# Performance work log

Hardware: AMD Instinct MI355X
Metric: run time of the kernel (lower is better)

Reference implementation:

```python
import jax, jax.numpy as jnp
import numpy as np

WS = 8  # window size (hardcoded in original forward)

def _window_partition(x, ws=WS):
    b, c, h, w = x.shape
    ph = (-h) % ws
    pw = (-w) % ws
    x = jnp.pad(x, ((0, 0), (0, 0), (0, ph), (0, pw)), mode='reflect')
    H, W = h + ph, w + pw
    # matches torch .view(b,c,ws,H//ws,ws,W//ws).permute(0,1,2,4,3,5)
    x = x.reshape(b, c, ws, H // ws, ws, W // ws)
    x = x.transpose(0, 1, 2, 4, 3, 5).reshape(b, c * ws * ws, H // ws, W // ws)
    return x, h, w, c, H // ws

def _l2norm_dim1(x):
    # F.normalize(x, p=2) defaults to dim=1 (token axis for [b, L, d]), eps=1e-12
    n = jnp.sqrt(jnp.sum(x * x, axis=1, keepdims=True))
    return x / jnp.maximum(n, 1e-12)

def _forward(q, k, v):
    b = q.shape[0]
    qp, qh, qw, qc, patch = _window_partition(q)
    kp, _, _, _, _ = _window_partition(k)
    vp, _, _, _, _ = _window_partition(v)
    d = qp.shape[1]  # c * ws * ws
    qt = qp.transpose(0, 2, 3, 1).reshape(b, -1, d)  # [b, L, d]
    kt = kp.transpose(0, 2, 3, 1).reshape(b, -1, d)
    vt = vp.transpose(0, 2, 3, 1).reshape(b, -1, d)
    _q = _l2norm_dim1(qt)
    _k = _l2norm_dim1(kt)
    _v = _l2norm_dim1(vt)
    sim = jnp.einsum('bld,bmd->blm', _q, _k) * (d ** -0.5)  # [b, L, L]
    out = jnp.einsum('blm,bmd->bld', jax.nn.softmax(sim, axis=-1), _v)
    # window_reverse
    L = out.shape[1]
    ws = WS
    x = out.reshape(b, patch, L // patch, qc, ws, ws)
    x = x.transpose(0, 3, 4, 1, 5, 2)  # (b, c, ws, patch, ws, L//patch)
    H = ws * patch
    x = x.reshape(b, qc, H, -1)
    return x[:, :, :qh, :qw]

def setup_inputs() -> dict:
    key = jax.random.key(0)
    kq, kk, kv = jax.random.split(key, 3)
    shape = (8, 32, 252, 252)
    return {
        'q': jax.random.normal(kq, shape, dtype=jnp.float32),
        'k': jax.random.normal(kk, shape, dtype=jnp.float32),
        'v': jax.random.normal(kv, shape, dtype=jnp.float32),
    }

def reference(q, k, v):
    return _forward(q, k, v)
```

## Files before the change

### kernel.cpp

```cpp
#include <hip/hip_runtime.h>
#include <cstdint>
#include <cstddef>


typedef __bf16 bf16x8 __attribute__((ext_vector_type(8)));
typedef float  f32x4  __attribute__((ext_vector_type(4)));

__device__ __forceinline__ unsigned int f2bf(float f) {
  unsigned int u = __builtin_bit_cast(unsigned int, f);
  u += 0x7FFFu + ((u >> 16) & 1u);
  return u >> 16;
}
__device__ __forceinline__ float bf2f(unsigned int h) {
  return __builtin_bit_cast(float, h << 16);
}

__device__ __forceinline__ void load_lds16(const void* g, void* l) {
  __builtin_amdgcn_global_load_lds(
      (const __attribute__((address_space(1))) void*)g,
      (__attribute__((address_space(3))) void*)l, 16, 0, 0);
}

__global__ __launch_bounds__(512)
void pack_qk_fused(const float* __restrict__ q, const float* __restrict__ k,
                   unsigned short* __restrict__ Qh,
                   unsigned short* __restrict__ Kh) {
  int bx  = blockIdx.x;
  int t   = bx >> 9;
  int b   = (bx >> 6) & 7;
  int i0  = (bx >> 3) & 7;
  int j0  = bx & 7;
  const float* xb = (t ? k : q) + (size_t)b * 32 * 63504;

  __shared__ unsigned short tile[1024 * 36];
  __shared__ float red[512];
  __shared__ float sclt[32];

  int tid = threadIdx.x;
  int ch  = tid & 7;
  int i1h = (tid >> 3) & 1;
  int c   = tid >> 4;

  int wbase = j0 * 32 + ch * 4;
  float we[4];
  #pragma unroll
  for (int e = 0; e < 4; e++) {
    int w = wbase + e;
    we[e] = (w >= 252) ? 0.f : (((unsigned)(w - 247) <= 3u) ? 2.f : 1.f);
  }
  bool tail = (wbase == 252);

  float pa = 0.f;
  unsigned short* X = (t ? Kh : Qh) + (size_t)b * 1024 * 2048;
  const float* csrc = xb + (size_t)c * 63504;

  #pragma unroll 4
  for (int r = 0; r < 16; r++) {
    int i1 = i1h * 16 + r;
    int h  = i0 * 32 + i1;
    int hs = (h < 252) ? h : 502 - h;
    float rw = (h >= 252) ? 0.f : (((unsigned)(h - 247) <= 3u) ? 2.f : 1.f);
    const float* rowp = csrc + (size_t)hs * 252;

    float4 vv;
    if (!tail) {
      vv = *(const float4*)&rowp[wbase];
    } else {
      vv.x = rowp[250]; vv.y = rowp[249]; vv.z = rowp[248]; vv.w = rowp[247];
    }
    pa += rw * (we[0] * vv.x * vv.x + we[1] * vv.y * vv.y +
                we[2] * vv.z * vv.z + we[3] * vv.w * vv.w);
    int lbase = i1 * 32 + ch * 4;
    unsigned short* tp = &tile[(size_t)lbase * 36 + c];
    tp[0]   = (unsigned short)f2bf(vv.x);
    tp[36]  = (unsigned short)f2bf(vv.y);
    tp[72]  = (unsigned short)f2bf(vv.z);
    tp[108] = (unsigned short)f2bf(vv.w);
  }
  __syncthreads();

  red[tid] = pa;
  __syncthreads();
  if (tid < 32) {
    float s = 0.f;
    #pragma unroll
    for (int u = 0; u < 16; u++) s += red[tid * 16 + u];
    sclt[tid] = 1.f / fmaxf(sqrtf(s), 1e-12f);
  }
  __syncthreads();

  {
    int qd   = tid & 7;
    int lidx = tid >> 3;
    float sc[4];
    #pragma unroll
    for (int m = 0; m < 4; m++) sc[m] = sclt[qd * 4 + m];
    unsigned short* Xb = &X[i0 * 256 + j0 * 32 + qd * 4];
    #pragma unroll 4
    for (int it = 0; it < 16; it++) {
      int l = it * 64 + lidx;
      uint2 u = *(const uint2*)&tile[(size_t)l * 36 + qd * 4];
      uint2 o2;
      o2.x = f2bf(bf2f(u.x & 0xFFFF) * sc[0]) |
             (f2bf(bf2f(u.x >> 16)   * sc[1]) << 16);
      o2.y = f2bf(bf2f(u.y & 0xFFFF) * sc[2]) |
             (f2bf(bf2f(u.y >> 16)   * sc[3]) << 16);
      *(uint2*)&Xb[(size_t)l * 2048] = o2;
    }
  }
}

__global__ void pack_v_kernel(const float* __restrict__ v,
                              unsigned short* __restrict__ Vt,
                              float* __restrict__ svsum) {
  int bx = blockIdx.x;
  int b  = bx >> 8;
  int i0 = (bx >> 5) & 7;
  int i1 = bx & 31;
  int h  = i0 * 32 + i1;
  int hs = (h < 252) ? h : 502 - h;
  const float* src = v + (size_t)b * 32 * 63504 + (size_t)hs * 252;
  unsigned short* dst = Vt + (size_t)b * 2048 * 1024
                           + (size_t)(i0 * 256) * 1024 + i1 * 32;

  int tid = threadIdx.x;
  int j1c = tid & 3;
  int c   = (tid >> 2) & 31;
  int j0g = tid >> 7;
  const float* s = src + (size_t)c * 63504;

  float psum[4];

  #pragma unroll
  for (int jj = 0; jj < 4; jj++) {
    int j0 = j0g * 4 + jj;
    int w0 = j0 * 32 + j1c * 8;
    float f0, f1, f2, f3, f4, f5, f6, f7;
    if (w0 + 8 <= 252) {
      float4 a = *(const float4*)&s[w0];
      float4 bq = *(const float4*)&s[w0 + 4];
      f0 = a.x; f1 = a.y; f2 = a.z; f3 = a.w;
      f4 = bq.x; f5 = bq.y; f6 = bq.z; f7 = bq.w;
    } else {
      float4 a = *(const float4*)&s[244];
      float4 bq = *(const float4*)&s[248];
      f0 = bq.x; f1 = bq.y; f2 = bq.z; f3 = bq.w;
      f4 = bq.z; f5 = bq.y; f6 = bq.x; f7 = a.w;
    }
    psum[jj] = f0*f0 + f1*f1 + f2*f2 + f3*f3 + f4*f4 + f5*f5 + f6*f6 + f7*f7;
    uint4 o;
    o.x = f2bf(f0) | (f2bf(f1) << 16);
    o.y = f2bf(f2) | (f2bf(f3) << 16);
    o.z = f2bf(f4) | (f2bf(f5) << 16);
    o.w = f2bf(f6) | (f2bf(f7) << 16);
    *(uint4*)&dst[(size_t)(j0 * 32 + c) * 1024 + j1c * 8] = o;
  }

  #pragma unroll
  for (int jj = 0; jj < 4; jj++) {
    float ssum = psum[jj];
    ssum += __shfl_down(ssum, 2, 4);
    ssum += __shfl_down(ssum, 1, 4);
    if (j1c == 0) {
      int j0 = j0g * 4 + jj;
      atomicAdd(&svsum[(size_t)b * 2048 + i0 * 256 + j0 * 32 + c], ssum);
    }
  }
}

template <int MODE>
__global__ __launch_bounds__(256, 4)
void gemm_nt(const unsigned short* __restrict__ A,
             const unsigned short* __restrict__ B,
             int K, int Asb, int Bsb, void* __restrict__ Cout, float scale,
             const float* __restrict__ sv) {
  __shared__ unsigned short lA[128 * 64];
  __shared__ unsigned short lB[128 * 64];
  __shared__ float svb[(MODE == 1) ? 128 : 1];

  const int flat = blockIdx.x;
  const int zz   = flat & 7;
  const int rr   = flat >> 3;
  const int my   = rr >> 3;
  const int nx   = rr & 7;

  const int tid  = threadIdx.x;
  const int lane = tid & 63;
  const int wave = tid >> 6;
  const int ln15 = lane & 15;
  const int q4   = lane >> 4;
  const int wm   = wave >> 1;
  const int wn   = wave & 1;
  const int m0   = my * 128;
  const int n0   = nx * 128;
  const unsigned short* Ab = A + (size_t)zz * Asb;
  const unsigned short* Bb = B + (size_t)zz * Bsb;

  if (MODE == 1 && tid < 128)
    svb[tid] = 1.f / fmaxf(sqrtf(sv[(size_t)zz * 2048 + m0 + tid]), 1e-12f);

  const int srow = lane >> 3;
  const int kcp  = lane & 7;
  const int kcl  = kcp ^ srow;

  f32x4 acc[4][4] = {};

  for (int k0 = 0; k0 < K; k0 += 64) {
    #pragma unroll
    for (int r = 0; r < 4; r++) {
      int rowg = wave * 32 + r * 8;
      int row  = rowg + srow;
      load_lds16(&Ab[(size_t)(m0 + row) * K + k0 + kcl * 8], &lA[rowg * 64]);
      load_lds16(&Bb[(size_t)(n0 + row) * K + k0 + kcl * 8], &lB[rowg * 64]);
    }
    __syncthreads();
    #pragma unroll
    for (int kk = 0; kk < 2; kk++) {
      bf16x8 af[4], bfr[4];
      #pragma unroll
      for (int mt = 0; mt < 4; mt++) {
        int row = wm * 64 + mt * 16 + ln15;
        int pc  = (kk * 4 + q4) ^ (row & 7);
        af[mt] = *(const bf16x8*)&lA[row * 64 + pc * 8];
      }
      #pragma unroll
      for (int nt = 0; nt < 4; nt++) {
        int row = wn * 64 + nt * 16 + ln15;
        int pc  = (kk * 4 + q4) ^ (row & 7);
        bfr[nt] = *(const bf16x8*)&lB[row * 64 + pc * 8];
      }
      #pragma unroll
      for (int mt = 0; mt < 4; mt++)
        #pragma unroll
        for (int nt = 0; nt < 4; nt++)
          acc[mt][nt] = __builtin_amdgcn_mfma_f32_16x16x32_bf16(
              af[mt], bfr[nt], acc[mt][nt], 0, 0, 0);
    }
    __syncthreads();
  }

  if (MODE == 0) {
    unsigned short* Sb = (unsigned short*)Cout + (size_t)zz * 1024 * 1024;
    #pragma unroll
    for (int mt = 0; mt < 4; mt++) {
      #pragma unroll
      for (int nt = 0; nt < 4; nt++) {
        int col = n0 + wn * 64 + nt * 16 + ln15;
        #pragma unroll
        for (int rg = 0; rg < 4; rg++) {
          int rowi = m0 + wm * 64 + mt * 16 + q4 * 4 + rg;
          Sb[(size_t)rowi * 1024 + col] = (unsigned short)f2bf(acc[mt][nt][rg] * scale);
        }
      }
    }
  } else {
    float* Ob = (float*)Cout;
    #pragma unroll
    for (int mt = 0; mt < 4; mt++) {
      #pragma unroll
      for (int nt = 0; nt < 4; nt++) {
        int l  = n0 + wn * 64 + nt * 16 + ln15;
        int i1 = l >> 5, j1 = l & 31;
        #pragma unroll
        for (int rg = 0; rg < 4; rg++) {
          int rloc = wm * 64 + mt * 16 + q4 * 4 + rg;
          int dp = m0 + rloc;
          int c  = dp & 31;
          int j0 = (dp >> 5) & 7;
          int i0 = dp >> 8;
          int h = i0 * 32 + i1;
          int w = j0 * 32 + j1;
          if (h < 252 && w < 252)
            Ob[(((size_t)zz * 32 + c) * 252 + h) * 252 + w] =
                acc[mt][nt][rg] * svb[rloc];
        }
      }
    }
  }
}

__global__ void softmax_kernel(unsigned short* __restrict__ S) {
  unsigned short* row = S + (size_t)blockIdx.x * 1024;
  int tid  = threadIdx.x;
  int lane = tid & 63;
  int wid  = tid >> 6;

  uint2 u = *(const uint2*)&row[tid * 4];
  float x0 = bf2f(u.x & 0xFFFF);
  float x1 = bf2f(u.x >> 16);
  float x2 = bf2f(u.y & 0xFFFF);
  float x3 = bf2f(u.y >> 16);

  __shared__ float red[8];
  float mx = fmaxf(fmaxf(x0, x1), fmaxf(x2, x3));
  #pragma unroll
  for (int off = 32; off > 0; off >>= 1) mx = fmaxf(mx, __shfl_down(mx, off));
  if (lane == 0) red[wid] = mx;
  __syncthreads();
  if (tid == 0)
    red[4] = fmaxf(fmaxf(red[0], red[1]), fmaxf(red[2], red[3]));
  __syncthreads();
  float bm = red[4];

  float e0 = __expf(x0 - bm), e1 = __expf(x1 - bm);
  float e2 = __expf(x2 - bm), e3 = __expf(x3 - bm);
  float s = e0 + e1 + e2 + e3;
  #pragma unroll
  for (int off = 32; off > 0; off >>= 1) s += __shfl_down(s, off);
  if (lane == 0) red[wid] = s;
  __syncthreads();
  if (tid == 0) red[5] = 1.0f / (red[0] + red[1] + red[2] + red[3]);
  __syncthreads();
  float inv = red[5];

  unsigned int o0 = f2bf(e0 * inv) | (f2bf(e1 * inv) << 16);
  unsigned int o1 = f2bf(e2 * inv) | (f2bf(e3 * inv) << 16);
  uint2 o; o.x = o0; o.y = o1;
  *(uint2*)&row[tid * 4] = o;
}

extern "C" void kernel_launch(void* const* d_in, const int* in_sizes, int n_in,
                              void* d_out, int out_size, void* d_ws, size_t ws_size,
                              hipStream_t stream) {
  const float* q = (const float*)d_in[0];
  const float* k = (const float*)d_in[1];
  const float* v = (const float*)d_in[2];
  float* out = (float*)d_out;

  char* ws = (char*)d_ws;
  float* sv = (float*)ws;
  unsigned short* Qh = (unsigned short*)(ws + 196608);
  unsigned short* Kh = Qh + (size_t)8 * 1024 * 2048;
  unsigned short* Vt = Kh + (size_t)8 * 1024 * 2048;
  unsigned short* S  = Vt + (size_t)8 * 2048 * 1024;

  const float SIM_SCALE = 0.02209708691207961f;

  hipMemsetAsync(sv, 0, (size_t)8 * 2048 * sizeof(float), stream);
  pack_qk_fused<<<1024, 512, 0, stream>>>(q, k, Qh, Kh);
  pack_v_kernel<<<2048, 256, 0, stream>>>(v, Vt, sv);
  gemm_nt<0><<<512, 256, 0, stream>>>(
      Qh, Kh, 2048, 1024 * 2048, 1024 * 2048, (void*)S, SIM_SCALE, nullptr);
  softmax_kernel<<<8192, 256, 0, stream>>>(S);
  gemm_nt<1><<<1024, 256, 0, stream>>>(
      Vt, S, 1024, 2048 * 1024, 1024 * 1024, (void*)out, 1.0f, sv);
}
```

Baseline: 356.3 us.

## Fuse softmax into QK^T GEMM epilogue and defer normalization to PV GEMM

Removes the standalone softmax kernel. The QK^T GEMM epilogue now writes exp(scaled score) without max subtraction and accumulates per-row sums with shuffles plus atomics. The PV GEMM divides its outputs by those row sums in its own epilogue. This saves one full read and write pass over the 8x1024x1024 score matrix and a kernel launch. In exchange it relies on scores being bounded, which holds here because the inputs are L2-normalized and scaled, and it adds atomic contention on the row-sum buffer.

```diff
diff --git a/kernel.cpp b/kernel.cpp
--- a/kernel.cpp
+++ b/kernel.cpp
@@ -173,10 +173,11 @@
 void gemm_nt(const unsigned short* __restrict__ A,
              const unsigned short* __restrict__ B,
              int K, int Asb, int Bsb, void* __restrict__ Cout, float scale,
-             const float* __restrict__ sv) {
+             const float* __restrict__ sv, float* __restrict__ rs) {
   __shared__ unsigned short lA[128 * 64];
   __shared__ unsigned short lB[128 * 64];
   __shared__ float svb[(MODE == 1) ? 128 : 1];
+  __shared__ float rsb[(MODE == 1) ? 128 : 1];
 
   const int flat = blockIdx.x;
   const int zz   = flat & 7;
@@ -196,8 +197,10 @@
   const unsigned short* Ab = A + (size_t)zz * Asb;
   const unsigned short* Bb = B + (size_t)zz * Bsb;
 
-  if (MODE == 1 && tid < 128)
+  if (MODE == 1 && tid < 128) {
     svb[tid] = 1.f / fmaxf(sqrtf(sv[(size_t)zz * 2048 + m0 + tid]), 1e-12f);
+    rsb[tid] = 1.f / rs[(size_t)zz * 1024 + n0 + tid];
+  }
 
   const int srow = lane >> 3;
   const int kcp  = lane & 7;
@@ -244,13 +247,22 @@
     #pragma unroll
     for (int mt = 0; mt < 4; mt++) {
       #pragma unroll
-      for (int nt = 0; nt < 4; nt++) {
-        int col = n0 + wn * 64 + nt * 16 + ln15;
+      for (int rg = 0; rg < 4; rg++) {
+        int rowi = m0 + wm * 64 + mt * 16 + q4 * 4 + rg;
+        float s = 0.f;
         #pragma unroll
-        for (int rg = 0; rg < 4; rg++) {
-          int rowi = m0 + wm * 64 + mt * 16 + q4 * 4 + rg;
-          Sb[(size_t)rowi * 1024 + col] = (unsigned short)f2bf(acc[mt][nt][rg] * scale);
+        for (int nt = 0; nt < 4; nt++) {
+          float e = __expf(acc[mt][nt][rg] * scale);
+          s += e;
+          int col = n0 + wn * 64 + nt * 16 + ln15;
+          Sb[(size_t)rowi * 1024 + col] = (unsigned short)f2bf(e);
         }
+        s += __shfl_xor(s, 1, 16);
+        s += __shfl_xor(s, 2, 16);
+        s += __shfl_xor(s, 4, 16);
+        s += __shfl_xor(s, 8, 16);
+        if (ln15 == 0)
+          atomicAdd(&rs[(size_t)zz * 1024 + rowi], s);
       }
     }
   } else {
@@ -259,8 +271,10 @@
     for (int mt = 0; mt < 4; mt++) {
       #pragma unroll
       for (int nt = 0; nt < 4; nt++) {
-        int l  = n0 + wn * 64 + nt * 16 + ln15;
+        int lcol = wn * 64 + nt * 16 + ln15;
+        int l  = n0 + lcol;
         int i1 = l >> 5, j1 = l & 31;
+        float rv = rsb[lcol];
         #pragma unroll
         for (int rg = 0; rg < 4; rg++) {
           int rloc = wm * 64 + mt * 16 + q4 * 4 + rg;
@@ -272,51 +286,11 @@
           int w = j0 * 32 + j1;
           if (h < 252 && w < 252)
             Ob[(((size_t)zz * 32 + c) * 252 + h) * 252 + w] =
-                acc[mt][nt][rg] * svb[rloc];
+                acc[mt][nt][rg] * svb[rloc] * rv;
         }
       }
     }
   }
-}
-
-__global__ void softmax_kernel(unsigned short* __restrict__ S) {
-  unsigned short* row = S + (size_t)blockIdx.x * 1024;
-  int tid  = threadIdx.x;
-  int lane = tid & 63;
-  int wid  = tid >> 6;
-
-  uint2 u = *(const uint2*)&row[tid * 4];
-  float x0 = bf2f(u.x & 0xFFFF);
-  float x1 = bf2f(u.x >> 16);
-  float x2 = bf2f(u.y & 0xFFFF);
-  float x3 = bf2f(u.y >> 16);
-
-  __shared__ float red[8];
-  float mx = fmaxf(fmaxf(x0, x1), fmaxf(x2, x3));
-  #pragma unroll
-  for (int off = 32; off > 0; off >>= 1) mx = fmaxf(mx, __shfl_down(mx, off));
-  if (lane == 0) red[wid] = mx;
-  __syncthreads();
-  if (tid == 0)
-    red[4] = fmaxf(fmaxf(red[0], red[1]), fmaxf(red[2], red[3]));
-  __syncthreads();
-  float bm = red[4];
-
-  float e0 = __expf(x0 - bm), e1 = __expf(x1 - bm);
-  float e2 = __expf(x2 - bm), e3 = __expf(x3 - bm);
-  float s = e0 + e1 + e2 + e3;
-  #pragma unroll
-  for (int off = 32; off > 0; off >>= 1) s += __shfl_down(s, off);
-  if (lane == 0) red[wid] = s;
-  __syncthreads();
-  if (tid == 0) red[5] = 1.0f / (red[0] + red[1] + red[2] + red[3]);
-  __syncthreads();
-  float inv = red[5];
-
-  unsigned int o0 = f2bf(e0 * inv) | (f2bf(e1 * inv) << 16);
-  unsigned int o1 = f2bf(e2 * inv) | (f2bf(e3 * inv) << 16);
-  uint2 o; o.x = o0; o.y = o1;
-  *(uint2*)&row[tid * 4] = o;
 }
 
 extern "C" void kernel_launch(void* const* d_in, const int* in_sizes, int n_in,
@@ -329,6 +303,7 @@
 
   char* ws = (char*)d_ws;
   float* sv = (float*)ws;
+  float* rsum = (float*)(ws + 65536);
   unsigned short* Qh = (unsigned short*)(ws + 196608);
   unsigned short* Kh = Qh + (size_t)8 * 1024 * 2048;
   unsigned short* Vt = Kh + (size_t)8 * 1024 * 2048;
@@ -336,12 +311,12 @@
 
   const float SIM_SCALE = 0.02209708691207961f;
 
-  hipMemsetAsync(sv, 0, (size_t)8 * 2048 * sizeof(float), stream);
+  hipMemsetAsync(sv, 0, 98304, stream);
   pack_qk_fused<<<1024, 512, 0, stream>>>(q, k, Qh, Kh);
   pack_v_kernel<<<2048, 256, 0, stream>>>(v, Vt, sv);
   gemm_nt<0><<<512, 256, 0, stream>>>(
-      Qh, Kh, 2048, 1024 * 2048, 1024 * 2048, (void*)S, SIM_SCALE, nullptr);
-  softmax_kernel<<<8192, 256, 0, stream>>>(S);
+      Qh, Kh, 2048, 1024 * 2048, 1024 * 2048, (void*)S, SIM_SCALE, nullptr,
+      rsum);
   gemm_nt<1><<<1024, 256, 0, stream>>>(
-      Vt, S, 1024, 2048 * 1024, 1024 * 1024, (void*)out, 1.0f, sv);
-}
+      Vt, S, 1024, 2048 * 1024, 1024 * 1024, (void*)out, 1.0f, sv, rsum);
+}
```

Result: no change. 350.1 us (-1.7%).
